# Kernel tuning notes

Hardware: AMD Instinct MI355X
Metric: run time of the kernel (lower is better)

Reference implementation:

```python
import jax, jax.numpy as jnp
import numpy as np

D_MODEL = 1024
NUM_HEADS = 16
HEAD_DIM = D_MODEL // NUM_HEADS


def setup_inputs() -> dict:
    key = jax.random.key(0)
    ks = jax.random.split(key, 5)
    B, S = 4, 2048
    scale = 0.02
    return {
        "x": jax.random.normal(ks[0], (B, S, D_MODEL), dtype=jnp.float32),
        "q_proj_weight": jax.random.normal(ks[1], (D_MODEL, D_MODEL), dtype=jnp.float32) * scale,
        "k_proj_weight": jax.random.normal(ks[2], (D_MODEL, D_MODEL), dtype=jnp.float32) * scale,
        "v_proj_weight": jax.random.normal(ks[3], (D_MODEL, D_MODEL), dtype=jnp.float32) * scale,
        "o_proj_weight": jax.random.normal(ks[4], (D_MODEL, D_MODEL), dtype=jnp.float32) * scale,
    }


def reference(x, q_proj_weight, k_proj_weight, v_proj_weight, o_proj_weight):
    B, S, _ = x.shape
    H, Dh = NUM_HEADS, HEAD_DIM

    def proj(w):  # [B,S,d_model] x [d_k,d_in] -> [B,H,S,Dh]
        p = jnp.einsum('bsd,kd->bsk', x, w)
        return p.reshape(B, S, H, Dh).transpose(0, 2, 1, 3)

    q = proj(q_proj_weight)
    k = proj(k_proj_weight)
    v = proj(v_proj_weight)

    scores = jnp.einsum('bhqd,bhkd->bhqk', q, k) / jnp.sqrt(jnp.asarray(Dh, dtype=x.dtype))
    causal = jnp.tril(jnp.ones((S, S), dtype=bool))  # [S,S]
    scores = jnp.where(causal, scores, -jnp.inf)
    attn = jax.nn.softmax(scores, axis=-1)
    out = jnp.einsum('bhqk,bhkd->bhqd', attn, v)  # [B,H,S,Dh]
    out = out.transpose(0, 2, 1, 3).reshape(B, S, D_MODEL)
    return jnp.einsum('bsv,mv->bsm', out, o_proj_weight)
```

## Files before the change

### kernel.cpp

```cpp
#include <hip/hip_runtime.h>
#include <cstdint>
#include <cstddef>

#define NH 16
#define DH 64
#define SEQ 2048
#define DM 1024

typedef __attribute__((ext_vector_type(8))) short short8;
typedef __attribute__((ext_vector_type(4))) float f32x4;

__device__ __forceinline__ unsigned short f2bf(float f) {
  unsigned u = __builtin_bit_cast(unsigned, f);
  u += 0x7fffu + ((u >> 16) & 1u);
  return (unsigned short)(u >> 16);
}

__device__ __forceinline__ void gld_lds16(const void* g, void* l) {
  __builtin_amdgcn_global_load_lds((const __attribute__((address_space(1))) void*)g,
                                   (__attribute__((address_space(3))) void*)l,
                                   16, 0, 0);
}

__global__ __launch_bounds__(256) void cast_all_kernel(const float* __restrict__ x,
                                                       const float* __restrict__ wq,
                                                       const float* __restrict__ wk,
                                                       const float* __restrict__ wv,
                                                       const float* __restrict__ wo,
                                                       unsigned short* __restrict__ xb,
                                                       unsigned short* __restrict__ wqkvb,
                                                       unsigned short* __restrict__ wob) {
  const int bid = blockIdx.x;
  const float* in;
  unsigned short* out;
  int i;
  if (bid < 8192) {
    in = x; out = xb; i = bid * 256 + threadIdx.x;
  } else {
    const int w = (bid - 8192) >> 10;
    i = ((bid - 8192) & 1023) * 256 + threadIdx.x;
    in = (w == 0) ? wq : (w == 1) ? wk : (w == 2) ? wv : wo;
    out = (w < 3) ? (wqkvb + (size_t)w * 1048576) : wob;
  }
  const float4 v = ((const float4*)in)[i];
  ushort4 o;
  o.x = f2bf(v.x); o.y = f2bf(v.y); o.z = f2bf(v.z); o.w = f2bf(v.w);
  ((ushort4*)out)[i] = o;
}

__global__ __launch_bounds__(256, 4) void gemm_qkv(const unsigned short* __restrict__ A,
                                                   const unsigned short* __restrict__ W,
                                                   unsigned short* __restrict__ qb,
                                                   unsigned short* __restrict__ kb,
                                                   unsigned short* __restrict__ vtb) {
  __shared__ __align__(16) unsigned short As[128 * 32];
  __shared__ __align__(16) unsigned short Bs[128 * 32];
  const int t = threadIdx.x;
  const int lane = t & 63;
  const int wave = t >> 6;
  const int quad = lane >> 4;
  const int l16 = lane & 15;
  const int wm = (wave >> 1) * 64;
  const int wn = (wave & 1) * 64;

  const int lid = blockIdx.x + 24 * blockIdx.y;
  const int xcd = lid & 7;
  const int idx = lid >> 3;
  const int bm = (xcd * 8 + idx / 24) * 128;
  const int bn = (idx % 24) * 128;
  const int sel = bn >> 10;
  const int bnl = bn & 1023;

  f32x4 acc[4][4];
#pragma unroll
  for (int i = 0; i < 4; ++i)
#pragma unroll
    for (int j = 0; j < 4; ++j) acc[i][j] = {0.0f, 0.0f, 0.0f, 0.0f};

  const int srow = t >> 2;
  const int sc = (t & 3) ^ ((srow >> 1) & 3);
  const unsigned short* Ag1 = A + (size_t)(bm + srow) * DM + sc * 8;
  const unsigned short* Ag2 = A + (size_t)(bm + srow + 64) * DM + sc * 8;
  const unsigned short* Bg1 = W + (size_t)(bn + srow) * DM + sc * 8;
  const unsigned short* Bg2 = W + (size_t)(bn + srow + 64) * DM + sc * 8;
  const int swz = (l16 >> 1) & 3;

  for (int k0 = 0; k0 < DM; k0 += 32) {
    __syncthreads();
    gld_lds16(Ag1 + k0, As + t * 8);
    gld_lds16(Ag2 + k0, As + t * 8 + 2048);
    gld_lds16(Bg1 + k0, Bs + t * 8);
    gld_lds16(Bg2 + k0, Bs + t * 8 + 2048);
    __syncthreads();
    short8 af[4], bfr[4];
#pragma unroll
    for (int i = 0; i < 4; ++i)
      af[i] = *(const short8*)(As + (wm + i * 16 + l16) * 32 + ((quad ^ swz) * 8));
#pragma unroll
    for (int j = 0; j < 4; ++j)
      bfr[j] = *(const short8*)(Bs + (wn + j * 16 + l16) * 32 + ((quad ^ swz) * 8));
#pragma unroll
    for (int i = 0; i < 4; ++i)
#pragma unroll
      for (int j = 0; j < 4; ++j)
        acc[i][j] = __builtin_amdgcn_mfma_f32_16x16x32_bf16(af[i], bfr[j], acc[i][j], 0, 0, 0);
  }

#pragma unroll
  for (int i = 0; i < 4; ++i) {
#pragma unroll
    for (int j = 0; j < 4; ++j) {
#pragma unroll
      for (int r = 0; r < 4; ++r) {
        const int m = bm + wm + i * 16 + quad * 4 + r;
        const int n = bnl + wn + j * 16 + l16;
        const float v = acc[i][j][r];
        if (sel == 0) {
          qb[(size_t)m * DM + n] = f2bf(v * 0.125f);
        } else if (sel == 1) {
          kb[(size_t)m * DM + n] = f2bf(v);
        } else {
          const int bb = m >> 11, s = m & 2047;
          const int h = n >> 6, d = n & 63;
          vtb[((size_t)((bb * NH + h) * DH + d)) * SEQ + s] = f2bf(v);
        }
      }
    }
  }
}

__global__ __launch_bounds__(256, 4) void gemm_o(const unsigned short* __restrict__ A,
                                                 const unsigned short* __restrict__ B,
                                                 float* __restrict__ C) {
  __shared__ __align__(16) unsigned short As[128 * 32];
  __shared__ __align__(16) unsigned short Bs[128 * 32];
  const int t = threadIdx.x;
  const int lane = t & 63;
  const int wave = t >> 6;
  const int quad = lane >> 4;
  const int l16 = lane & 15;
  const int wm = (wave >> 1) * 64;
  const int wn = (wave & 1) * 64;

  const int lid = blockIdx.x + 8 * blockIdx.y;
  const int xcd = lid & 7;
  const int idx = lid >> 3;
  const int bm = (xcd * 8 + idx / 8) * 128;
  const int bn = (idx % 8) * 128;

  f32x4 acc[4][4];
#pragma unroll
  for (int i = 0; i < 4; ++i)
#pragma unroll
    for (int j = 0; j < 4; ++j) acc[i][j] = {0.0f, 0.0f, 0.0f, 0.0f};

  const int srow = t >> 2;
  const int sc = (t & 3) ^ ((srow >> 1) & 3);
  const unsigned short* Ag1 = A + (size_t)(bm + srow) * DM + sc * 8;
  const unsigned short* Ag2 = A + (size_t)(bm + srow + 64) * DM + sc * 8;
  const unsigned short* Bg1 = B + (size_t)(bn + srow) * DM + sc * 8;
  const unsigned short* Bg2 = B + (size_t)(bn + srow + 64) * DM + sc * 8;
  const int swz = (l16 >> 1) & 3;

  for (int k0 = 0; k0 < DM; k0 += 32) {
    __syncthreads();
    gld_lds16(Ag1 + k0, As + t * 8);
    gld_lds16(Ag2 + k0, As + t * 8 + 2048);
    gld_lds16(Bg1 + k0, Bs + t * 8);
    gld_lds16(Bg2 + k0, Bs + t * 8 + 2048);
    __syncthreads();
    short8 af[4], bfr[4];
#pragma unroll
    for (int i = 0; i < 4; ++i)
      af[i] = *(const short8*)(As + (wm + i * 16 + l16) * 32 + ((quad ^ swz) * 8));
#pragma unroll
    for (int j = 0; j < 4; ++j)
      bfr[j] = *(const short8*)(Bs + (wn + j * 16 + l16) * 32 + ((quad ^ swz) * 8));
#pragma unroll
    for (int i = 0; i < 4; ++i)
#pragma unroll
      for (int j = 0; j < 4; ++j)
        acc[i][j] = __builtin_amdgcn_mfma_f32_16x16x32_bf16(af[i], bfr[j], acc[i][j], 0, 0, 0);
  }

#pragma unroll
  for (int i = 0; i < 4; ++i)
#pragma unroll
    for (int j = 0; j < 4; ++j)
#pragma unroll
      for (int r = 0; r < 4; ++r) {
        const int m = bm + wm + i * 16 + quad * 4 + r;
        const int n = bn + wn + j * 16 + l16;
        C[(size_t)m * DM + n] = acc[i][j][r];
      }
}

__global__ __launch_bounds__(512) void attn_kernel(const unsigned short* __restrict__ Q,
                                                   const unsigned short* __restrict__ K,
                                                   const unsigned short* __restrict__ Vt,
                                                   unsigned short* __restrict__ O) {
  __shared__ __align__(16) unsigned short Ks[128 * 64];
  __shared__ __align__(16) unsigned short Vs[64 * 128];
  __shared__ __align__(16) unsigned short Ps[8][16 * 136];
  const int t = threadIdx.x;
  const int lane = t & 63;
  const int wave = t >> 6;
  const int quad = lane >> 4;
  const int l16 = lane & 15;
  const int h = blockIdx.y;
  const int b = blockIdx.z;

  const int ksr1 = t >> 3;
  const int ksr2 = (t + 512) >> 3;
  const int koff1 = (b * SEQ + ksr1) * DM + h * 64 + (((t & 7) ^ (ksr1 & 7)) * 8);
  const int koff2 = (b * SEQ + ksr2) * DM + h * 64 + (((t & 7) ^ (ksr2 & 7)) * 8);
  const int vsr1 = t >> 4;
  const int vsr2 = (t + 512) >> 4;
  const int voff1 = ((b * NH + h) * DH + vsr1) * SEQ + (((t & 15) ^ (vsr1 & 15)) * 8);
  const int voff2 = ((b * NH + h) * DH + vsr2) * SEQ + (((t & 15) ^ (vsr2 & 15)) * 8);
  unsigned short* Pw = &Ps[wave][0];
  const int swz = l16 & 7;

#pragma unroll 1
  for (int pass = 0; pass < 2; ++pass) {
    const int qt = (pass == 0) ? (int)blockIdx.x : 15 - (int)blockIdx.x;
    const int qtile = qt * 128;
    const int row_lo = qtile + wave * 16;
    const int row_hi = row_lo + 15;

    const unsigned short* Qrow =
        Q + ((size_t)(b * SEQ + row_lo + l16)) * DM + h * 64;
    const short8 qf0 = *(const short8*)(Qrow + quad * 8);
    const short8 qf1 = *(const short8*)(Qrow + 32 + quad * 8);

    f32x4 o_acc[4];
#pragma unroll
    for (int nb = 0; nb < 4; ++nb) o_acc[nb] = {0.0f, 0.0f, 0.0f, 0.0f};
    float l_r[4] = {0.0f, 0.0f, 0.0f, 0.0f};

    const int ktiles = qt + 1;
    for (int kt = 0; kt < ktiles; ++kt) {
      const int kbase = kt * 128;
      __syncthreads();
      gld_lds16(K + koff1 + (size_t)kbase * DM, Ks + t * 8);
      gld_lds16(K + koff2 + (size_t)kbase * DM, Ks + (t + 512) * 8);
      gld_lds16(Vt + voff1 + kbase, Vs + t * 8);
      gld_lds16(Vt + voff2 + kbase, Vs + (t + 512) * 8);
      __syncthreads();

      if (kbase <= row_hi) {
        f32x4 s_acc[8];
#pragma unroll
        for (int nb = 0; nb < 8; ++nb) {
          s_acc[nb] = {0.0f, 0.0f, 0.0f, 0.0f};
          const short8 kf0 = *(const short8*)(Ks + (nb * 16 + l16) * 64 + ((quad ^ swz) * 8));
          const short8 kf1 = *(const short8*)(Ks + (nb * 16 + l16) * 64 + (((4 | quad) ^ swz) * 8));
          s_acc[nb] = __builtin_amdgcn_mfma_f32_16x16x32_bf16(qf0, kf0, s_acc[nb], 0, 0, 0);
          s_acc[nb] = __builtin_amdgcn_mfma_f32_16x16x32_bf16(qf1, kf1, s_acc[nb], 0, 0, 0);
        }

        const bool need_mask = (kbase + 127 > row_lo);
#pragma unroll
        for (int r = 0; r < 4; ++r) {
          const int qr = row_lo + quad * 4 + r;
#pragma unroll
          for (int nb = 0; nb < 8; ++nb) {
            float p = __expf(s_acc[nb][r]);
            if (need_mask) p = ((kbase + nb * 16 + l16) <= qr) ? p : 0.0f;
            l_r[r] += p;
            const unsigned u = __builtin_bit_cast(unsigned, p);
            Pw[(quad * 4 + r) * 136 + nb * 16 + l16] =
                (unsigned short)((u + 0x8000u) >> 16);
          }
        }

#pragma unroll
        for (int kk = 0; kk < 4; ++kk) {
          const short8 pf = *(const short8*)(Pw + l16 * 136 + kk * 32 + quad * 8);
#pragma unroll
          for (int nb = 0; nb < 4; ++nb) {
            const short8 vf = *(const short8*)(Vs + (nb * 16 + l16) * 128 +
                                               (((kk * 4 + quad) ^ l16) * 8));
            o_acc[nb] = __builtin_amdgcn_mfma_f32_16x16x32_bf16(pf, vf, o_acc[nb], 0, 0, 0);
          }
        }
      }
    }

#pragma unroll
    for (int r = 0; r < 4; ++r) {
      float ls = l_r[r];
      ls += __shfl_xor(ls, 1);
      ls += __shfl_xor(ls, 2);
      ls += __shfl_xor(ls, 4);
      ls += __shfl_xor(ls, 8);
      const float inv_l = 1.0f / ls;
      const int qr = row_lo + quad * 4 + r;
#pragma unroll
      for (int nb = 0; nb < 4; ++nb)
        O[((size_t)(b * SEQ + qr)) * DM + h * 64 + nb * 16 + l16] =
            f2bf(o_acc[nb][r] * inv_l);
    }
  }
}

extern "C" void kernel_launch(void* const* d_in, const int* in_sizes, int n_in,
                              void* d_out, int out_size, void* d_ws, size_t ws_size,
                              hipStream_t stream) {
  const float* x  = (const float*)d_in[0];
  const float* wq = (const float*)d_in[1];
  const float* wk = (const float*)d_in[2];
  const float* wv = (const float*)d_in[3];
  const float* wo = (const float*)d_in[4];

  char* ws = (char*)d_ws;
  unsigned short* xb    = (unsigned short*)(ws);
  unsigned short* wqkvb = (unsigned short*)(ws + 16777216);
  unsigned short* wob   = (unsigned short*)(ws + 23068672);
  unsigned short* qb    = (unsigned short*)(ws + 25165824);
  unsigned short* kb    = (unsigned short*)(ws + 41943040);
  unsigned short* vtb   = (unsigned short*)(ws + 58720256);
  unsigned short* aob   = (unsigned short*)(ws + 75497472);

  cast_all_kernel<<<12288, 256, 0, stream>>>(x, wq, wk, wv, wo, xb, wqkvb, wob);

  gemm_qkv<<<dim3(24, 64), 256, 0, stream>>>(xb, wqkvb, qb, kb, vtb);

  attn_kernel<<<dim3(8, NH, 4), 512, 0, stream>>>(qb, kb, vtb, aob);

  gemm_o<<<dim3(8, 64), 256, 0, stream>>>(aob, wob, (float*)d_out);
}
```

Baseline: 273.7 us.

## Rewrite QKV GEMM with 256x256 tiles and a 4-stage async LDS pipeline

Replaces the 128x128 QKV projection GEMM with a 512-thread, 256x256-tile kernel that uses a 4-deep ring of LDS buffers filled by global_load_lds. Loads for tile t+3 are issued between the MFMA groups, with s_waitcnt vmcnt and s_setprio used to overlap memory with compute and to drop one of the two barriers per k-step. The larger tile raises reuse per loaded byte. In exchange it needs 128KB of dynamic LDS, which limits occupancy to one block per CU, and the grid shrinks to 384 blocks, which may leave CUs poorly balanced.

```diff
diff --git a/kernel.cpp b/kernel.cpp
--- a/kernel.cpp
+++ b/kernel.cpp
@@ -48,66 +48,118 @@
   ((ushort4*)out)[i] = o;
 }
 
-__global__ __launch_bounds__(256, 4) void gemm_qkv(const unsigned short* __restrict__ A,
-                                                   const unsigned short* __restrict__ W,
-                                                   unsigned short* __restrict__ qb,
-                                                   unsigned short* __restrict__ kb,
-                                                   unsigned short* __restrict__ vtb) {
-  __shared__ __align__(16) unsigned short As[128 * 32];
-  __shared__ __align__(16) unsigned short Bs[128 * 32];
+__global__ __launch_bounds__(512, 2) void gemm_qkv256(const unsigned short* __restrict__ A,
+                                                      const unsigned short* __restrict__ W,
+                                                      unsigned short* __restrict__ qb,
+                                                      unsigned short* __restrict__ kb,
+                                                      unsigned short* __restrict__ vtb) {
+  extern __shared__ __align__(16) unsigned short smem[];
+  unsigned short* As = smem;
+  unsigned short* Bs = smem + 4 * 8192;
+
   const int t = threadIdx.x;
   const int lane = t & 63;
   const int wave = t >> 6;
   const int quad = lane >> 4;
   const int l16 = lane & 15;
-  const int wm = (wave >> 1) * 64;
-  const int wn = (wave & 1) * 64;
-
-  const int lid = blockIdx.x + 24 * blockIdx.y;
-  const int xcd = lid & 7;
-  const int idx = lid >> 3;
-  const int bm = (xcd * 8 + idx / 24) * 128;
-  const int bn = (idx % 24) * 128;
+  const int wm = (wave >> 2) * 128;
+  const int wn = (wave & 3) * 64;
+
+  const int bid = blockIdx.x;
+  const int xcd = bid & 7;
+  const int idx = bid >> 3;
+  const int bm = (xcd * 4 + idx / 12) * 256;
+  const int bn = (idx % 12) * 256;
   const int sel = bn >> 10;
   const int bnl = bn & 1023;
 
-  f32x4 acc[4][4];
-#pragma unroll
-  for (int i = 0; i < 4; ++i)
+  f32x4 acc[8][4];
+#pragma unroll
+  for (int i = 0; i < 8; ++i)
 #pragma unroll
     for (int j = 0; j < 4; ++j) acc[i][j] = {0.0f, 0.0f, 0.0f, 0.0f};
 
-  const int srow = t >> 2;
-  const int sc = (t & 3) ^ ((srow >> 1) & 3);
-  const unsigned short* Ag1 = A + (size_t)(bm + srow) * DM + sc * 8;
-  const unsigned short* Ag2 = A + (size_t)(bm + srow + 64) * DM + sc * 8;
-  const unsigned short* Bg1 = W + (size_t)(bn + srow) * DM + sc * 8;
-  const unsigned short* Bg2 = W + (size_t)(bn + srow + 64) * DM + sc * 8;
+  const int r0 = t >> 2;
+  const int c0 = (((t & 3) ^ ((r0 >> 1) & 3)) * 8);
+  const unsigned short* Ag0 = A + (size_t)(bm + r0) * DM + c0;
+  const unsigned short* Ag1 = A + (size_t)(bm + r0 + 128) * DM + c0;
+  const unsigned short* Bg0 = W + (size_t)(bn + r0) * DM + c0;
+  const unsigned short* Bg1 = W + (size_t)(bn + r0 + 128) * DM + c0;
+
+#define STAGE_A(tt)                                                  \
+  {                                                                  \
+    unsigned short* d = As + ((tt) & 3) * 8192 + t * 8;              \
+    gld_lds16(Ag0 + (tt) * 32, d);                                   \
+    gld_lds16(Ag1 + (tt) * 32, d + 4096);                            \
+  }
+#define STAGE_B(tt)                                                  \
+  {                                                                  \
+    unsigned short* d = Bs + ((tt) & 3) * 8192 + t * 8;              \
+    gld_lds16(Bg0 + (tt) * 32, d);                                   \
+    gld_lds16(Bg1 + (tt) * 32, d + 4096);                            \
+  }
+
   const int swz = (l16 >> 1) & 3;
-
-  for (int k0 = 0; k0 < DM; k0 += 32) {
-    __syncthreads();
-    gld_lds16(Ag1 + k0, As + t * 8);
-    gld_lds16(Ag2 + k0, As + t * 8 + 2048);
-    gld_lds16(Bg1 + k0, Bs + t * 8);
-    gld_lds16(Bg2 + k0, Bs + t * 8 + 2048);
-    __syncthreads();
-    short8 af[4], bfr[4];
-#pragma unroll
-    for (int i = 0; i < 4; ++i)
-      af[i] = *(const short8*)(As + (wm + i * 16 + l16) * 32 + ((quad ^ swz) * 8));
-#pragma unroll
-    for (int j = 0; j < 4; ++j)
-      bfr[j] = *(const short8*)(Bs + (wn + j * 16 + l16) * 32 + ((quad ^ swz) * 8));
-#pragma unroll
-    for (int i = 0; i < 4; ++i)
-#pragma unroll
-      for (int j = 0; j < 4; ++j)
-        acc[i][j] = __builtin_amdgcn_mfma_f32_16x16x32_bf16(af[i], bfr[j], acc[i][j], 0, 0, 0);
-  }
-
-#pragma unroll
-  for (int i = 0; i < 4; ++i) {
+  const int aoff = l16 * 32 + ((quad ^ swz) * 8);
+
+#define QKV_TILE(tt, DO_STAGE)                                                             \
+  {                                                                                        \
+    const unsigned short* Ab = As + ((tt) & 3) * 8192;                                     \
+    const unsigned short* Bb = Bs + ((tt) & 3) * 8192;                                     \
+    short8 af[4], bfr[4];                                                                  \
+    _Pragma("unroll")                                                                      \
+    for (int i = 0; i < 4; ++i)                                                            \
+      af[i] = *(const short8*)(Ab + (wm + i * 16) * 32 + aoff);                            \
+    _Pragma("unroll")                                                                      \
+    for (int j = 0; j < 4; ++j)                                                            \
+      bfr[j] = *(const short8*)(Bb + (wn + j * 16) * 32 + aoff);                           \
+    if (DO_STAGE) { STAGE_A((tt) + 3); }                                                   \
+    __builtin_amdgcn_s_setprio(1);                                                         \
+    _Pragma("unroll")                                                                      \
+    for (int i = 0; i < 4; ++i)                                                            \
+      _Pragma("unroll")                                                                    \
+      for (int j = 0; j < 4; ++j)                                                          \
+        acc[i][j] = __builtin_amdgcn_mfma_f32_16x16x32_bf16(af[i], bfr[j], acc[i][j], 0, 0, 0); \
+    __builtin_amdgcn_s_setprio(0);                                                         \
+    _Pragma("unroll")                                                                      \
+    for (int i = 0; i < 4; ++i)                                                            \
+      af[i] = *(const short8*)(Ab + (wm + 64 + i * 16) * 32 + aoff);                       \
+    if (DO_STAGE) { STAGE_B((tt) + 3); }                                                   \
+    __builtin_amdgcn_s_setprio(1);                                                         \
+    _Pragma("unroll")                                                                      \
+    for (int i = 0; i < 4; ++i)                                                            \
+      _Pragma("unroll")                                                                    \
+      for (int j = 0; j < 4; ++j)                                                          \
+        acc[4 + i][j] = __builtin_amdgcn_mfma_f32_16x16x32_bf16(af[i], bfr[j], acc[4 + i][j], 0, 0, 0); \
+    __builtin_amdgcn_s_setprio(0);                                                         \
+  }
+
+  STAGE_A(0); STAGE_B(0);
+  STAGE_A(1); STAGE_B(1);
+  STAGE_A(2); STAGE_B(2);
+
+#pragma unroll 1
+  for (int tt = 0; tt < 30; ++tt) {
+    asm volatile("s_waitcnt vmcnt(8)" ::: "memory");
+    __builtin_amdgcn_s_barrier();
+    asm volatile("" ::: "memory");
+    QKV_TILE(tt, tt < 29);
+  }
+  asm volatile("s_waitcnt vmcnt(4)" ::: "memory");
+  __builtin_amdgcn_s_barrier();
+  asm volatile("" ::: "memory");
+  QKV_TILE(30, false);
+  asm volatile("s_waitcnt vmcnt(0)" ::: "memory");
+  __builtin_amdgcn_s_barrier();
+  asm volatile("" ::: "memory");
+  QKV_TILE(31, false);
+
+#undef QKV_TILE
+#undef STAGE_A
+#undef STAGE_B
+
+#pragma unroll
+  for (int i = 0; i < 8; ++i) {
 #pragma unroll
     for (int j = 0; j < 4; ++j) {
 #pragma unroll
@@ -322,9 +374,16 @@
   unsigned short* vtb   = (unsigned short*)(ws + 58720256);
   unsigned short* aob   = (unsigned short*)(ws + 75497472);
 
+  static bool s_attr_done = false;
+  if (!s_attr_done) {
+    hipFuncSetAttribute(reinterpret_cast<const void*>(gemm_qkv256),
+                        hipFuncAttributeMaxDynamicSharedMemorySize, 131072);
+    s_attr_done = true;
+  }
+
   cast_all_kernel<<<12288, 256, 0, stream>>>(x, wq, wk, wv, wo, xb, wqkvb, wob);
 
-  gemm_qkv<<<dim3(24, 64), 256, 0, stream>>>(xb, wqkvb, qb, kb, vtb);
+  gemm_qkv256<<<dim3(384), dim3(512), 131072, stream>>>(xb, wqkvb, qb, kb, vtb);
 
   attn_kernel<<<dim3(8, NH, 4), 512, 0, stream>>>(qb, kb, vtb, aob);
 
```

New measurement: 276.0 us. Within noise of the previous version (+0.8%).

## Double-buffer GEMM K-loop with direct-to-LDS A and register-prefetched B

Applied to the files above, without the earlier changes.

Rewrites both projection GEMMs around a shared core. It uses BK=64 tiles and double-buffered LDS for A, loaded with global_load_lds, while B fragments are prefetched straight from global memory into registers two tiles ahead. Explicit vmcnt waits, barriers and setprio let the MFMAs overlap the loads. The V-transpose epilogue now stages through LDS so the transposed stores are coalesced 16-byte writes. The trade-off is higher register pressure (occupancy hint lowered to 2) and B reads from global that are not shared across waves.

```diff
diff --git a/kernel.cpp b/kernel.cpp
--- a/kernel.cpp
+++ b/kernel.cpp
@@ -48,13 +48,86 @@
   ((ushort4*)out)[i] = o;
 }
 
-__global__ __launch_bounds__(256, 4) void gemm_qkv(const unsigned short* __restrict__ A,
-                                                   const unsigned short* __restrict__ W,
-                                                   unsigned short* __restrict__ qb,
-                                                   unsigned short* __restrict__ kb,
-                                                   unsigned short* __restrict__ vtb) {
-  __shared__ __align__(16) unsigned short As[128 * 32];
-  __shared__ __align__(16) unsigned short Bs[128 * 32];
+
+#define ST_A(T, PAR)                                                                     \
+  {                                                                                      \
+    gld_lds16(aSb + 0 * 32 * DM + (T) * 64, sm + (PAR) * 16384 + 0 * 4096 + t * 16);     \
+    gld_lds16(aSb + 1 * 32 * DM + (T) * 64, sm + (PAR) * 16384 + 1 * 4096 + t * 16);     \
+    gld_lds16(aSb + 2 * 32 * DM + (T) * 64, sm + (PAR) * 16384 + 2 * 4096 + t * 16);     \
+    gld_lds16(aSb + 3 * 32 * DM + (T) * 64, sm + (PAR) * 16384 + 3 * 4096 + t * 16);     \
+  }
+
+#define LD_B(DST, T)                                                                     \
+  _Pragma("unroll")                                                                      \
+  for (int j = 0; j < 4; ++j) {                                                          \
+    DST[j][0] = *(const short8*)(Bb + (size_t)j * 16 * DM + (T) * 64);                   \
+    DST[j][1] = *(const short8*)(Bb + (size_t)j * 16 * DM + (T) * 64 + 32);              \
+  }
+
+#define RD_A(PAR)                                                                        \
+  _Pragma("unroll")                                                                      \
+  for (int i = 0; i < 4; ++i) {                                                          \
+    af[i][0] = *(const short8*)(sm + (PAR) * 16384 + i * 2048 + aRd0);                   \
+    af[i][1] = *(const short8*)(sm + (PAR) * 16384 + i * 2048 + (aRd0 ^ 64));            \
+  }
+
+#define MMALL(BF)                                                                        \
+  _Pragma("unroll")                                                                      \
+  for (int i = 0; i < 4; ++i)                                                            \
+    _Pragma("unroll")                                                                    \
+    for (int j = 0; j < 4; ++j) {                                                        \
+      acc[i][j] = __builtin_amdgcn_mfma_f32_16x16x32_bf16(af[i][0], BF[j][0], acc[i][j], 0, 0, 0); \
+      acc[i][j] = __builtin_amdgcn_mfma_f32_16x16x32_bf16(af[i][1], BF[j][1], acc[i][j], 0, 0, 0); \
+    }
+
+#define GTILE(T, PAR, BF, DO_PRE)                                                        \
+  {                                                                                      \
+    if ((T) < 15) asm volatile("s_waitcnt vmcnt(12)" ::: "memory");                      \
+    else          asm volatile("s_waitcnt vmcnt(0)" ::: "memory");                       \
+    __builtin_amdgcn_s_barrier();                                                        \
+    asm volatile("" ::: "memory");                                                       \
+    RD_A(PAR);                                                                           \
+    asm volatile("s_waitcnt lgkmcnt(0)" ::: "memory");                                   \
+    __builtin_amdgcn_sched_barrier(0);                                                   \
+    __builtin_amdgcn_s_setprio(1);                                                       \
+    MMALL(BF);                                                                           \
+    __builtin_amdgcn_s_setprio(0);                                                       \
+    asm volatile("" ::: "memory");                                                       \
+    __builtin_amdgcn_s_barrier();                                                        \
+    if (DO_PRE) { ST_A((T) + 2, (PAR)); LD_B(BF, (T) + 2); }                             \
+  }
+
+#define GEMM_CORE()                                                                      \
+  f32x4 acc[4][4];                                                                       \
+  _Pragma("unroll")                                                                      \
+  for (int i = 0; i < 4; ++i)                                                            \
+    _Pragma("unroll")                                                                    \
+    for (int j = 0; j < 4; ++j) acc[i][j] = {0.0f, 0.0f, 0.0f, 0.0f};                    \
+  const int r0s = t >> 3;                                                                \
+  const int g0 = (((t & 7) ^ (r0s & 7)) * 8);                                            \
+  const unsigned short* aSb = Amat + (size_t)(bm + r0s) * DM + g0;                       \
+  const unsigned short* Bb = Bmat + (size_t)(bn + wn + l16) * DM + quad * 8;             \
+  const int aRd0 = (wm + l16) * 128 + ((quad ^ (l16 & 7)) * 16);                         \
+  short8 af[4][2], bfA[4][2], bfB[4][2];                                                 \
+  ST_A(0, 0);                                                                            \
+  LD_B(bfA, 0);                                                                          \
+  ST_A(1, 1);                                                                            \
+  LD_B(bfB, 1);                                                                          \
+  _Pragma("unroll 1")                                                                    \
+  for (int tp = 0; tp < 7; ++tp) {                                                       \
+    const int T0 = tp * 2;                                                               \
+    GTILE(T0, 0, bfA, 1)                                                                 \
+    GTILE(T0 + 1, 1, bfB, 1)                                                             \
+  }                                                                                      \
+  GTILE(14, 0, bfA, 0)                                                                   \
+  GTILE(15, 1, bfB, 0)
+
+__global__ __launch_bounds__(256, 2) void gemm_qkv128(const unsigned short* __restrict__ Amat,
+                                                      const unsigned short* __restrict__ Bmat,
+                                                      unsigned short* __restrict__ qb,
+                                                      unsigned short* __restrict__ kb,
+                                                      unsigned short* __restrict__ vtb) {
+  __shared__ __align__(16) char sm[32768];
   const int t = threadIdx.x;
   const int lane = t & 63;
   const int wave = t >> 6;
@@ -63,7 +136,7 @@
   const int wm = (wave >> 1) * 64;
   const int wn = (wave & 1) * 64;
 
-  const int lid = blockIdx.x + 24 * blockIdx.y;
+  const int lid = blockIdx.x;
   const int xcd = lid & 7;
   const int idx = lid >> 3;
   const int bm = (xcd * 8 + idx / 24) * 128;
@@ -71,69 +144,65 @@
   const int sel = bn >> 10;
   const int bnl = bn & 1023;
 
-  f32x4 acc[4][4];
-#pragma unroll
-  for (int i = 0; i < 4; ++i)
-#pragma unroll
-    for (int j = 0; j < 4; ++j) acc[i][j] = {0.0f, 0.0f, 0.0f, 0.0f};
-
-  const int srow = t >> 2;
-  const int sc = (t & 3) ^ ((srow >> 1) & 3);
-  const unsigned short* Ag1 = A + (size_t)(bm + srow) * DM + sc * 8;
-  const unsigned short* Ag2 = A + (size_t)(bm + srow + 64) * DM + sc * 8;
-  const unsigned short* Bg1 = W + (size_t)(bn + srow) * DM + sc * 8;
-  const unsigned short* Bg2 = W + (size_t)(bn + srow + 64) * DM + sc * 8;
-  const int swz = (l16 >> 1) & 3;
-
-  for (int k0 = 0; k0 < DM; k0 += 32) {
+  GEMM_CORE();
+
+  if (sel == 2) {
     __syncthreads();
-    gld_lds16(Ag1 + k0, As + t * 8);
-    gld_lds16(Ag2 + k0, As + t * 8 + 2048);
-    gld_lds16(Bg1 + k0, Bs + t * 8);
-    gld_lds16(Bg2 + k0, Bs + t * 8 + 2048);
+#pragma unroll
+    for (int i = 0; i < 4; ++i) {
+#pragma unroll
+      for (int j = 0; j < 4; ++j) {
+        const int n = wn + j * 16 + l16;
+        const int nrow = n * 256;
+        const int cswz = (n & 15) << 4;
+        const int mb = wm + i * 16 + quad * 4;
+#pragma unroll
+        for (int rp = 0; rp < 2; ++rp) {
+          const unsigned lo = f2bf(acc[i][j][rp * 2]);
+          const unsigned hi = f2bf(acc[i][j][rp * 2 + 1]);
+          const int m0 = mb + rp * 2;
+          *(unsigned*)(sm + nrow + ((2 * m0) ^ cswz)) = lo | (hi << 16);
+        }
+      }
+    }
     __syncthreads();
-    short8 af[4], bfr[4];
-#pragma unroll
-    for (int i = 0; i < 4; ++i)
-      af[i] = *(const short8*)(As + (wm + i * 16 + l16) * 32 + ((quad ^ swz) * 8));
-#pragma unroll
-    for (int j = 0; j < 4; ++j)
-      bfr[j] = *(const short8*)(Bs + (wn + j * 16 + l16) * 32 + ((quad ^ swz) * 8));
-#pragma unroll
-    for (int i = 0; i < 4; ++i)
-#pragma unroll
-      for (int j = 0; j < 4; ++j)
-        acc[i][j] = __builtin_amdgcn_mfma_f32_16x16x32_bf16(af[i], bfr[j], acc[i][j], 0, 0, 0);
-  }
-
-#pragma unroll
-  for (int i = 0; i < 4; ++i) {
-#pragma unroll
-    for (int j = 0; j < 4; ++j) {
-#pragma unroll
-      for (int r = 0; r < 4; ++r) {
-        const int m = bm + wm + i * 16 + quad * 4 + r;
-        const int n = bnl + wn + j * 16 + l16;
-        const float v = acc[i][j][r];
-        if (sel == 0) {
-          qb[(size_t)m * DM + n] = f2bf(v * 0.125f);
-        } else if (sel == 1) {
-          kb[(size_t)m * DM + n] = f2bf(v);
-        } else {
-          const int bb = m >> 11, s = m & 2047;
-          const int h = n >> 6, d = n & 63;
-          vtb[((size_t)((bb * NH + h) * DH + d)) * SEQ + s] = f2bf(v);
+    const int mc = t & 15;
+    const int nr = t >> 4;
+    const int bb = bm >> 11;
+    const int sbase = (bm & 2047) + mc * 8;
+#pragma unroll
+    for (int c = 0; c < 8; ++c) {
+      const int n = nr + c * 16;
+      const f32x4 v = *(const f32x4*)(sm + n * 256 + ((mc * 16) ^ (nr << 4)));
+      const int gn = bnl + n;
+      const int h = gn >> 6, d = gn & 63;
+      *(f32x4*)(vtb + ((size_t)((bb * NH + h) * DH + d)) * SEQ + sbase) = v;
+    }
+  } else {
+#pragma unroll
+    for (int i = 0; i < 4; ++i) {
+#pragma unroll
+      for (int j = 0; j < 4; ++j) {
+#pragma unroll
+        for (int r = 0; r < 4; ++r) {
+          const int m = bm + wm + i * 16 + quad * 4 + r;
+          const int n = bnl + wn + j * 16 + l16;
+          const float v = acc[i][j][r];
+          if (sel == 0) {
+            qb[(size_t)m * DM + n] = f2bf(v * 0.125f);
+          } else {
+            kb[(size_t)m * DM + n] = f2bf(v);
+          }
         }
       }
     }
   }
 }
 
-__global__ __launch_bounds__(256, 4) void gemm_o(const unsigned short* __restrict__ A,
-                                                 const unsigned short* __restrict__ B,
-                                                 float* __restrict__ C) {
-  __shared__ __align__(16) unsigned short As[128 * 32];
-  __shared__ __align__(16) unsigned short Bs[128 * 32];
+__global__ __launch_bounds__(256, 2) void gemm_o128(const unsigned short* __restrict__ Amat,
+                                                    const unsigned short* __restrict__ Bmat,
+                                                    float* __restrict__ C) {
+  __shared__ __align__(16) char sm[32768];
   const int t = threadIdx.x;
   const int lane = t & 63;
   const int wave = t >> 6;
@@ -142,46 +211,13 @@
   const int wm = (wave >> 1) * 64;
   const int wn = (wave & 1) * 64;
 
-  const int lid = blockIdx.x + 8 * blockIdx.y;
+  const int lid = blockIdx.x;
   const int xcd = lid & 7;
   const int idx = lid >> 3;
   const int bm = (xcd * 8 + idx / 8) * 128;
   const int bn = (idx % 8) * 128;
 
-  f32x4 acc[4][4];
-#pragma unroll
-  for (int i = 0; i < 4; ++i)
-#pragma unroll
-    for (int j = 0; j < 4; ++j) acc[i][j] = {0.0f, 0.0f, 0.0f, 0.0f};
-
-  const int srow = t >> 2;
-  const int sc = (t & 3) ^ ((srow >> 1) & 3);
-  const unsigned short* Ag1 = A + (size_t)(bm + srow) * DM + sc * 8;
-  const unsigned short* Ag2 = A + (size_t)(bm + srow + 64) * DM + sc * 8;
-  const unsigned short* Bg1 = B + (size_t)(bn + srow) * DM + sc * 8;
-  const unsigned short* Bg2 = B + (size_t)(bn + srow + 64) * DM + sc * 8;
-  const int swz = (l16 >> 1) & 3;
-
-  for (int k0 = 0; k0 < DM; k0 += 32) {
-    __syncthreads();
-    gld_lds16(Ag1 + k0, As + t * 8);
-    gld_lds16(Ag2 + k0, As + t * 8 + 2048);
-    gld_lds16(Bg1 + k0, Bs + t * 8);
-    gld_lds16(Bg2 + k0, Bs + t * 8 + 2048);
-    __syncthreads();
-    short8 af[4], bfr[4];
-#pragma unroll
-    for (int i = 0; i < 4; ++i)
-      af[i] = *(const short8*)(As + (wm + i * 16 + l16) * 32 + ((quad ^ swz) * 8));
-#pragma unroll
-    for (int j = 0; j < 4; ++j)
-      bfr[j] = *(const short8*)(Bs + (wn + j * 16 + l16) * 32 + ((quad ^ swz) * 8));
-#pragma unroll
-    for (int i = 0; i < 4; ++i)
-#pragma unroll
-      for (int j = 0; j < 4; ++j)
-        acc[i][j] = __builtin_amdgcn_mfma_f32_16x16x32_bf16(af[i], bfr[j], acc[i][j], 0, 0, 0);
-  }
+  GEMM_CORE();
 
 #pragma unroll
   for (int i = 0; i < 4; ++i)
@@ -324,9 +360,9 @@
 
   cast_all_kernel<<<12288, 256, 0, stream>>>(x, wq, wk, wv, wo, xb, wqkvb, wob);
 
-  gemm_qkv<<<dim3(24, 64), 256, 0, stream>>>(xb, wqkvb, qb, kb, vtb);
+  gemm_qkv128<<<dim3(1536), dim3(256), 0, stream>>>(xb, wqkvb, qb, kb, vtb);
 
   attn_kernel<<<dim3(8, NH, 4), 512, 0, stream>>>(qb, kb, vtb, aob);
 
-  gemm_o<<<dim3(8, 64), 256, 0, stream>>>(aob, wob, (float*)d_out);
-}
+  gemm_o128<<<dim3(512), dim3(256), 0, stream>>>(aob, wob, (float*)d_out);
+}
```

New measurement: 308.1 us. 12.6% more time.
